# Kernel optimization log

Hardware: AMD Instinct MI355X
Metric: run time of the kernel (lower is better)

## Reference

```python
import jax, jax.numpy as jnp
import numpy as np

N = 50000      # nodes
E = 800000     # edges (before self-loops)
IN = 128       # in_channels
HID = 32       # hidden_channels per head
H = 4          # in_head
OUT = 40       # out_channels
OH = 1         # out_head
NEG = 0.2      # GATConv default negative_slope
EPS = 1e-5     # BatchNorm eps
SKIP = 0.5     # skip_coefficient


def setup_inputs() -> dict:
    key = jax.random.key(0)
    ks = jax.random.split(key, 24)
    s = 0.1
    f32 = jnp.float32
    return dict(
        x=jax.random.normal(ks[0], (N, IN), dtype=f32),
        W0=jax.random.normal(ks[1], (H * HID, IN), dtype=f32) * s,
        as0=jax.random.normal(ks[2], (H, HID), dtype=f32) * s,
        ad0=jax.random.normal(ks[3], (H, HID), dtype=f32) * s,
        b0=jnp.zeros((H * HID,), f32),
        g0=jnp.ones((H * HID,), f32),
        be0=jnp.zeros((H * HID,), f32),
        W1=jax.random.normal(ks[4], (H * HID, H * HID), dtype=f32) * s,
        as1=jax.random.normal(ks[5], (H, HID), dtype=f32) * s,
        ad1=jax.random.normal(ks[6], (H, HID), dtype=f32) * s,
        b1=jnp.zeros((H * HID,), f32),
        g1=jnp.ones((H * HID,), f32),
        be1=jnp.zeros((H * HID,), f32),
        W2=jax.random.normal(ks[7], (OH * OUT, H * HID), dtype=f32) * s,
        as2=jax.random.normal(ks[8], (OH, OUT), dtype=f32) * s,
        ad2=jax.random.normal(ks[9], (OH, OUT), dtype=f32) * s,
        b2=jnp.zeros((OH * OUT,), f32),
        edge_index=jax.random.randint(ks[10], (2, E), 0, N, dtype=jnp.int64),
    )


def gat_layer(x, src, dst, W, a_s, a_d, b, heads, ch):
    # PyG GATConv (concat=True): per-head linear, edge LeakyReLU attention,
    # softmax over incoming edges per destination node, scatter-add aggregate.
    n = x.shape[0]
    h = (x @ W.T).reshape(n, heads, ch)            # [N,H,C]
    al_s = jnp.einsum('nhc,hc->nh', h, a_s)        # [N,H]
    al_d = jnp.einsum('nhc,hc->nh', h, a_d)
    e = jax.nn.leaky_relu(al_s[src] + al_d[dst], NEG)   # [Etot,H]
    m = jax.ops.segment_max(e, dst, num_segments=n)     # per-dst max (stable softmax)
    ex = jnp.exp(e - m[dst])
    denom = jax.ops.segment_sum(ex, dst, num_segments=n)
    alpha = ex / denom[dst]                              # [Etot,H]
    out = jax.ops.segment_sum(alpha[:, :, None] * h[src], dst, num_segments=n)
    return out.reshape(n, heads * ch) + b


def batchnorm(x, g, b):
    # BatchNorm1d, batch-statistics form
    mu = x.mean(0)
    var = x.var(0)
    return (x - mu) * jax.lax.rsqrt(var + EPS) * g + b


def reference(x, W0, as0, ad0, b0, g0, be0, W1, as1, ad1, b1, g1, be1,
              W2, as2, ad2, b2, edge_index):
    loops = jnp.arange(N, dtype=edge_index.dtype)   # GATConv add_self_loops=True
    src = jnp.concatenate([edge_index[0], loops])
    dst = jnp.concatenate([edge_index[1], loops])
    h = jax.nn.relu(batchnorm(gat_layer(x, src, dst, W0, as0, ad0, b0, H, HID), g0, be0))
    skip = h
    h = gat_layer(h, src, dst, W1, as1, ad1, b1, H, HID)
    h = jax.nn.relu(batchnorm(h, g1, be1) + SKIP * skip)
    return gat_layer(h, src, dst, W2, as2, ad2, b2, OH, OUT)
```

## Files before the change

### kernel.cpp

```cpp
#include <hip/hip_runtime.h>
#include <hip/hip_bf16.h>
#include <stdint.h>

#define N_NODES 50000
#define N_EDGES 800000
#define TOT_EDGES (N_EDGES + N_NODES)
#define DIM 128
#define NEG 0.2f
#define BN_EPS 1e-5f
#define SKIPC 0.5f
#define NB 196
#define BCAP 6144

typedef __attribute__((ext_vector_type(8))) short short8;
typedef __attribute__((ext_vector_type(4))) float f32x4;

__device__ inline float bf2f(__hip_bfloat16 v) { return __bfloat162float(v); }
__device__ inline float u16f(unsigned short u) { return __uint_as_float(((unsigned int)u) << 16); }
__device__ inline unsigned short f2bu(float f) {
    __hip_bfloat16 b = __float2bfloat16(f);
    return *(unsigned short*)&b;
}
__device__ inline void fma8(float* acc, float ex, uint4 u) {
    acc[0] += ex * u16f((unsigned short)(u.x & 0xFFFFu));
    acc[1] += ex * u16f((unsigned short)(u.x >> 16));
    acc[2] += ex * u16f((unsigned short)(u.y & 0xFFFFu));
    acc[3] += ex * u16f((unsigned short)(u.y >> 16));
    acc[4] += ex * u16f((unsigned short)(u.z & 0xFFFFu));
    acc[5] += ex * u16f((unsigned short)(u.z >> 16));
    acc[6] += ex * u16f((unsigned short)(u.w & 0xFFFFu));
    acc[7] += ex * u16f((unsigned short)(u.w >> 16));
}
__device__ inline unsigned int pk2(float a, float b) {
    return (unsigned int)f2bu(a) | ((unsigned int)f2bu(b) << 16);
}

__global__ void zero_out_k(unsigned short* out, int n) {
    int g = blockIdx.x * 256 + threadIdx.x;
    if (g < n) out[g] = 0;
}

__global__ void fdetect_k(const unsigned int* __restrict__ w0, int* __restrict__ fflag) {
    __shared__ int cs;
    if (threadIdx.x == 0) cs = 0;
    __syncthreads();
    unsigned int w = w0[threadIdx.x];
    float v0 = u16f((unsigned short)(w & 0xFFFFu));
    float a = fabsf(v0);
    int sane = (a < 2.0f && (a > 1e-20f || v0 == 0.0f)) ? 1 : 0;
    atomicAdd(&cs, sane);
    __syncthreads();
    if (threadIdx.x == 0) fflag[0] = (cs >= 128) ? 1 : 0;
}

__global__ __launch_bounds__(256) void binA_k(const int* __restrict__ ei,
                                              int* __restrict__ bcnt,
                                              unsigned int* __restrict__ pairs) {
    __shared__ int cnt[NB], base[NB], cur[NB];
    __shared__ int sf;
    int t = threadIdx.x;
    if (t == 0) sf = 0;
    for (int i = t; i < NB; i += 256) cnt[i] = 0;
    __syncthreads();
    if (t < 16 && ei[2 * t + 1] != 0) atomicOr(&sf, 1);
    __syncthreads();
    int f = (sf == 0);
    int b0 = blockIdx.x * 4096;
    unsigned int pk[16];
    int bk[16];
    #pragma unroll
    for (int j = 0; j < 16; ++j) {
        int g = b0 + j * 256 + t;
        bk[j] = -1;
        if (g < N_EDGES) {
            int s, d;
            if (f) { s = ei[2 * g]; d = ei[2 * (N_EDGES + g)]; }
            else   { s = ei[g];     d = ei[N_EDGES + g]; }
            if ((unsigned)d < N_NODES && (unsigned)s < N_NODES) {
                bk[j] = d >> 8;
                pk[j] = (unsigned int)s | ((unsigned int)(d & 255) << 16);
                atomicAdd(&cnt[bk[j]], 1);
            }
        }
    }
    __syncthreads();
    if (t < NB) {
        int c = cnt[t];
        base[t] = c ? atomicAdd(&bcnt[t], c) : 0;
        cur[t] = 0;
    }
    __syncthreads();
    #pragma unroll
    for (int j = 0; j < 16; ++j) {
        if (bk[j] >= 0) {
            int off = base[bk[j]] + atomicAdd(&cur[bk[j]], 1);
            if (off < BCAP) pairs[(size_t)bk[j] * BCAP + off] = pk[j];
        }
    }
}

__global__ __launch_bounds__(256) void bucketscan_k(const int* __restrict__ bcnt,
                                                    int* __restrict__ bbase,
                                                    int* __restrict__ row_ptr) {
    __shared__ int sm[256];
    int t = threadIdx.x;
    int v = 0;
    if (t < NB) {
        int nn = min(256, N_NODES - t * 256);
        v = min(bcnt[t], BCAP) + nn;
    }
    sm[t] = v;
    __syncthreads();
    for (int off = 1; off < 256; off <<= 1) {
        int x = (t >= off) ? sm[t - off] : 0;
        __syncthreads();
        sm[t] += x;
        __syncthreads();
    }
    if (t < NB) bbase[t] = sm[t] - v;
    if (t == 255) row_ptr[N_NODES] = sm[255];
}

__global__ __launch_bounds__(256) void binB_k(const int* __restrict__ bcnt,
                                              const int* __restrict__ bbase,
                                              const unsigned int* __restrict__ pairs,
                                              int* __restrict__ row_ptr,
                                              int* __restrict__ ssrc) {
    __shared__ int cntL[256], scanL[256], curL[256];
    int b = blockIdx.x, t = threadIdx.x;
    int n0 = b * 256;
    int nn = min(256, N_NODES - n0);
    int cnt_b = min(bcnt[b], BCAP);
    const unsigned int* P = pairs + (size_t)b * BCAP;
    cntL[t] = (t < nn) ? 1 : 0;
    __syncthreads();
    for (int i = t; i < cnt_b; i += 256)
        atomicAdd(&cntL[P[i] >> 16], 1);
    __syncthreads();
    int v = cntL[t];
    scanL[t] = v;
    __syncthreads();
    for (int off = 1; off < 256; off <<= 1) {
        int x = (t >= off) ? scanL[t - off] : 0;
        __syncthreads();
        scanL[t] += x;
        __syncthreads();
    }
    int excl = scanL[t] - v;
    int gbase = bbase[b];
    if (t < nn) row_ptr[n0 + t] = gbase + excl;
    curL[t] = excl;
    __syncthreads();
    if (t < nn) {
        int pos = atomicAdd(&curL[t], 1);
        ssrc[gbase + pos] = n0 + t;
    }
    for (int i = t; i < cnt_b; i += 256) {
        unsigned int p = P[i];
        int pos = atomicAdd(&curL[p >> 16], 1);
        ssrc[gbase + pos] = (int)(p & 0xFFFFu);
    }
}

struct PrepJobs { const void* src[13]; float* dst[13]; int n[13]; };
__global__ __launch_bounds__(256) void wcvt_k(const void* __restrict__ W0,
                                              const void* __restrict__ W1,
                                              const void* __restrict__ W2,
                                              unsigned short* __restrict__ Wb0,
                                              unsigned short* __restrict__ Wb1,
                                              unsigned short* __restrict__ Wb2,
                                              PrepJobs jobs,
                                              const int* __restrict__ fflag) {
    int f = fflag[0];
    int b = blockIdx.x;
    if (b < 148) {
        int g = b * 256 + threadIdx.x;
        const void* W; unsigned short* Wb; int idx;
        if (g < 16384)        { W = W0; Wb = Wb0; idx = g; }
        else if (g < 32768)   { W = W1; Wb = Wb1; idx = g - 16384; }
        else if (g < 37888)   { W = W2; Wb = Wb2; idx = g - 32768; }
        else return;
        if (f) Wb[idx] = ((const unsigned short*)W)[idx];
        else   Wb[idx] = f2bu(((const float*)W)[idx]);
    } else {
        int j = b - 148;
        int n = jobs.n[j];
        const void* s = jobs.src[j];
        float* d = jobs.dst[j];
        for (int i = threadIdx.x; i < n; i += 256)
            d[i] = f ? bf2f(((const __hip_bfloat16*)s)[i]) : ((const float*)s)[i];
    }
}

__global__ __launch_bounds__(256) void wext_k(unsigned short* __restrict__ Wb0,
                                              unsigned short* __restrict__ Wb1,
                                              unsigned short* __restrict__ Wb2,
                                              const float* __restrict__ pAs0, const float* __restrict__ pAd0,
                                              const float* __restrict__ pAs1, const float* __restrict__ pAd1,
                                              const float* __restrict__ pAs2, const float* __restrict__ pAd2) {
    int g = blockIdx.x * 256 + threadIdx.x;
    if (g < 2048) {
        int layer = g >> 10;
        int gi = g & 1023;
        int rowq = gi >> 7;
        int k = gi & 127;
        int hh = rowq & 3, dir = rowq >> 2;
        unsigned short* Wb = layer ? Wb1 : Wb0;
        const float* p = layer ? (dir ? pAd1 : pAs1) : (dir ? pAd0 : pAs0);
        float v = 0.f;
        #pragma unroll
        for (int c = 0; c < 32; ++c)
            v += p[hh * 32 + c] * u16f(Wb[(size_t)(hh * 32 + c) * 128 + k]);
        Wb[(size_t)(128 + dir * 4 + hh) * 128 + k] = f2bu(v);
    } else if (g < 2304) {
        int gi = g - 2048;
        int dir = gi >> 7;
        int k = gi & 127;
        const float* p = dir ? pAd2 : pAs2;
        float v = 0.f;
        #pragma unroll
        for (int c = 0; c < 40; ++c)
            v += p[c] * u16f(Wb2[(size_t)c * 128 + k]);
        Wb2[(size_t)(40 + dir) * 128 + k] = f2bu(v);
    }
}

template<int MT, int MV, int ALBASE, int NH, bool BF16IN>
__device__ inline void mfma_body(const unsigned short* __restrict__ Xb,
                                 const float* __restrict__ Xf,
                                 const unsigned short* __restrict__ Wb,
                                 unsigned short* __restrict__ Y,
                                 float* __restrict__ als, float* __restrict__ ald, int n) {
    const int MROWS = ALBASE + 2 * NH;
    int wave = (blockIdx.x * blockDim.x + threadIdx.x) >> 6;
    int r0 = wave * 16;
    if (r0 >= n) return;
    int lane = threadIdx.x & 63;
    int m = lane & 15, quad = lane >> 4;
    f32x4 acc[MT];
    #pragma unroll
    for (int t = 0; t < MT; ++t) acc[t] = (f32x4){0.f, 0.f, 0.f, 0.f};
    int arow = min(r0 + m, n - 1);

    #pragma unroll
    for (int kc = 0; kc < 4; ++kc) {
        int k0 = kc * 32 + quad * 8;
        short8 a;
        if (BF16IN) {
            a = *(const short8*)(Xb + (size_t)arow * 128 + k0);
        } else {
            const float* xp = Xf + (size_t)arow * 128 + k0;
            float4 x0 = *(const float4*)xp;
            float4 x1 = *(const float4*)(xp + 4);
            a[0] = (short)f2bu(x0.x); a[1] = (short)f2bu(x0.y);
            a[2] = (short)f2bu(x0.z); a[3] = (short)f2bu(x0.w);
            a[4] = (short)f2bu(x1.x); a[5] = (short)f2bu(x1.y);
            a[6] = (short)f2bu(x1.z); a[7] = (short)f2bu(x1.w);
        }
        #pragma unroll
        for (int t = 0; t < MT; ++t) {
            int col = t * 16 + m;
            short8 b;
            if (col < MROWS) b = *(const short8*)(Wb + (size_t)col * 128 + k0);
            else             b = (short8){0,0,0,0,0,0,0,0};
            acc[t] = __builtin_amdgcn_mfma_f32_16x16x32_bf16(a, b, acc[t], 0, 0, 0);
        }
    }

    #pragma unroll
    for (int t = 0; t < MT; ++t) {
        int col = t * 16 + m;
        #pragma unroll
        for (int r = 0; r < 4; ++r) {
            int row = r0 + quad * 4 + r;
            if (row >= n) continue;
            if (col < MV) {
                Y[(size_t)row * MV + col] = f2bu(acc[t][r]);
            } else if (col < ALBASE + NH) {
                als[row * NH + (col - ALBASE)] = acc[t][r];
            } else if (col < ALBASE + 2 * NH) {
                ald[row * NH + (col - ALBASE - NH)] = acc[t][r];
            }
        }
    }
}

__global__ __launch_bounds__(256) void mfma_x_k(const void* __restrict__ X,
                                                const unsigned short* __restrict__ Wb,
                                                unsigned short* __restrict__ Y,
                                                float* __restrict__ als, float* __restrict__ ald,
                                                int n, const int* __restrict__ fflag) {
    if (fflag[0]) mfma_body<9, 128, 128, 4, true>((const unsigned short*)X, nullptr, Wb, Y, als, ald, n);
    else          mfma_body<9, 128, 128, 4, false>(nullptr, (const float*)X, Wb, Y, als, ald, n);
}

__global__ __launch_bounds__(256) void mfma_b_k(const unsigned short* __restrict__ X,
                                                const unsigned short* __restrict__ Wb,
                                                unsigned short* __restrict__ Y,
                                                float* __restrict__ als, float* __restrict__ ald, int n) {
    mfma_body<9, 128, 128, 4, true>(X, nullptr, Wb, Y, als, ald, n);
}

__global__ __launch_bounds__(256) void mfma_b40_k(const unsigned short* __restrict__ X,
                                                  const unsigned short* __restrict__ Wb,
                                                  unsigned short* __restrict__ Y,
                                                  float* __restrict__ als, float* __restrict__ ald, int n) {
    mfma_body<3, 40, 40, 1, true>(X, nullptr, Wb, Y, als, ald, n);
}

template<int H, int C, int LPG, int CPL, bool FINAL>
__global__ __launch_bounds__(256) void agg4_k(const unsigned short* __restrict__ hbuf,
                                              const float* __restrict__ als,
                                              const float* __restrict__ ald,
                                              const float* __restrict__ bias,
                                              const int* __restrict__ row_ptr,
                                              const int* __restrict__ ssrc,
                                              void* __restrict__ out,
                                              const int* __restrict__ fflag, int n) {
    const int HC = H * C;
    const int G = 64 / LPG;
    const int NV = CPL / 8;
    int gw = (blockIdx.x * blockDim.x + threadIdx.x) >> 6;
    if (gw >= n) return;
    int lane = threadIdx.x & 63;
    int grp = lane / LPG;
    int sl  = lane % LPG;
    int c0 = sl * CPL;
    bool act = c0 < HC;
    int hl = act ? (c0 / C) : 0;
    int d = gw;
    int beg = row_ptr[d], end = row_ptr[d + 1];
    float adh = ald[d * H + hl];

    float denom = 0.f;
    float acc[CPL];
    #pragma unroll
    for (int j = 0; j < CPL; ++j) acc[j] = 0.f;

    int i0 = beg + grp;
    bool h0 = i0 < end;
    bool h1 = (i0 + G) < end;
    float al0 = 0.f, al1 = 0.f;
    uint4 u0[NV], u1[NV];
    if (h0) {
        int s = ssrc[i0];
        al0 = als[s * H + hl];
        if (act) {
            const uint4* hp = (const uint4*)(hbuf + (size_t)s * HC + c0);
            #pragma unroll
            for (int v = 0; v < NV; ++v) u0[v] = hp[v];
        }
    }
    if (h1) {
        int s = ssrc[i0 + G];
        al1 = als[s * H + hl];
        if (act) {
            const uint4* hp = (const uint4*)(hbuf + (size_t)s * HC + c0);
            #pragma unroll
            for (int v = 0; v < NV; ++v) u1[v] = hp[v];
        }
    }
    int inext = i0 + 2 * G;

    while (h0) {
        bool h2 = inext < end;
        float al2 = 0.f;
        uint4 u2[NV];
        if (h2) {
            int s = ssrc[inext];
            al2 = als[s * H + hl];
            if (act) {
                const uint4* hp = (const uint4*)(hbuf + (size_t)s * HC + c0);
                #pragma unroll
                for (int v = 0; v < NV; ++v) u2[v] = hp[v];
            }
        }
        float t = al0 + adh;
        t = t > 0.f ? t : NEG * t;
        float ex = __expf(t);
        denom += ex;
        if (act) {
            #pragma unroll
            for (int v = 0; v < NV; ++v) fma8(acc + v * 8, ex, u0[v]);
        }
        h0 = h1; al0 = al1;
        #pragma unroll
        for (int v = 0; v < NV; ++v) u0[v] = u1[v];
        h1 = h2; al1 = al2;
        #pragma unroll
        for (int v = 0; v < NV; ++v) u1[v] = u2[v];
        inext += G;
    }

    #pragma unroll
    for (int off = LPG; off < 64; off <<= 1) {
        denom += __shfl_xor(denom, off, 64);
        #pragma unroll
        for (int j = 0; j < CPL; ++j) acc[j] += __shfl_xor(acc[j], off, 64);
    }

    if (grp == 0 && act) {
        float inv = 1.f / denom;
        float vals[CPL];
        #pragma unroll
        for (int j = 0; j < CPL; ++j) vals[j] = acc[j] * inv + bias[c0 + j];
        if (FINAL && !fflag[0]) {
            float* of = (float*)out + (size_t)d * HC + c0;
            #pragma unroll
            for (int j = 0; j < CPL; ++j) of[j] = vals[j];
        } else {
            unsigned short* ob = (unsigned short*)out + (size_t)d * HC + c0;
            #pragma unroll
            for (int v = 0; v < NV; ++v) {
                uint4 pk;
                pk.x = pk2(vals[v * 8 + 0], vals[v * 8 + 1]);
                pk.y = pk2(vals[v * 8 + 2], vals[v * 8 + 3]);
                pk.z = pk2(vals[v * 8 + 4], vals[v * 8 + 5]);
                pk.w = pk2(vals[v * 8 + 6], vals[v * 8 + 7]);
                *(uint4*)(ob + v * 8) = pk;
            }
        }
    }
}

__global__ __launch_bounds__(256) void bn_stats_k(const unsigned short* __restrict__ x,
                                                  float* __restrict__ sum,
                                                  float* __restrict__ sumsq, int n) {
    __shared__ float ss[256], sq[256];
    int t = threadIdx.x;
    int c = t & 127, half = t >> 7;
    float s = 0.f, s2 = 0.f;
    for (int r = blockIdx.x * 2 + half; r < n; r += gridDim.x * 2) {
        float v = u16f(x[(size_t)r * 128 + c]);
        s += v; s2 += v * v;
    }
    ss[t] = s; sq[t] = s2;
    __syncthreads();
    if (t < 128) {
        s = ss[t] + ss[t + 128];
        s2 = sq[t] + sq[t + 128];
        atomicAdd(&sum[c], s);
        atomicAdd(&sumsq[c], s2);
    }
}

__global__ void bn_apply_k(const unsigned short* __restrict__ x,
                           const unsigned short* __restrict__ skip,
                           unsigned short* __restrict__ y,
                           const float* __restrict__ sum, const float* __restrict__ sumsq,
                           const float* __restrict__ g, const float* __restrict__ be, int n) {
    int gid = blockIdx.x * 256 + threadIdx.x;
    if (gid >= n * 32) return;
    int e0 = gid * 4;
    int c0 = e0 & 127;
    const float invN = 1.f / (float)N_NODES;
    float4 gg = *(const float4*)(g + c0);
    float4 bb = *(const float4*)(be + c0);
    float4 sm = *(const float4*)(sum + c0);
    float4 sq = *(const float4*)(sumsq + c0);
    ushort4 xv = *(const ushort4*)(x + e0);
    float vx[4] = { u16f(xv.x), u16f(xv.y), u16f(xv.z), u16f(xv.w) };
    float mg[4] = { gg.x, gg.y, gg.z, gg.w };
    float mb[4] = { bb.x, bb.y, bb.z, bb.w };
    float ms[4] = { sm.x, sm.y, sm.z, sm.w };
    float mq[4] = { sq.x, sq.y, sq.z, sq.w };
    float sk[4] = { 0.f, 0.f, 0.f, 0.f };
    if (skip) {
        ushort4 sv = *(const ushort4*)(skip + e0);
        sk[0] = u16f(sv.x); sk[1] = u16f(sv.y); sk[2] = u16f(sv.z); sk[3] = u16f(sv.w);
    }
    unsigned short o[4];
    #pragma unroll
    for (int j = 0; j < 4; ++j) {
        float mean = ms[j] * invN;
        float var = fmaxf(mq[j] * invN - mean * mean, 0.f);
        float inv = rsqrtf(var + BN_EPS);
        float v = (vx[j] - mean) * inv * mg[j] + mb[j];
        if (skip) v += SKIPC * sk[j];
        o[j] = f2bu(fmaxf(v, 0.f));
    }
    *(ushort4*)(y + e0) = make_ushort4(o[0], o[1], o[2], o[3]);
}

extern "C" void kernel_launch(void* const* d_in, const int* in_sizes, int n_in,
                              void* d_out, int out_size, void* d_ws, size_t ws_size,
                              hipStream_t stream) {
    const void* x   = d_in[0];
    const void* W0  = d_in[1];
    const void* as0 = d_in[2];
    const void* ad0 = d_in[3];
    const void* b0  = d_in[4];
    const void* g0  = d_in[5];
    const void* be0 = d_in[6];
    const void* W1  = d_in[7];
    const void* as1 = d_in[8];
    const void* ad1 = d_in[9];
    const void* b1  = d_in[10];
    const void* g1  = d_in[11];
    const void* be1 = d_in[12];
    const void* W2  = d_in[13];
    const void* as2 = d_in[14];
    const void* ad2 = d_in[15];
    const void* b2  = d_in[16];
    const int* ei = (const int*)d_in[17];

    char* w = (char*)d_ws;
    size_t off = 0;
    auto alloc = [&](size_t bytes) -> void* {
        void* p = w + off;
        off = (off + bytes + 255) & ~(size_t)255;
        return p;
    };
    unsigned short* hAgg = (unsigned short*)alloc((size_t)N_NODES * 128 * 2);
    unsigned short* hbf  = (unsigned short*)alloc((size_t)N_NODES * 128 * 2);
    unsigned short* hS   = (unsigned short*)alloc((size_t)N_NODES * 128 * 2);
    unsigned short* hI   = (unsigned short*)alloc((size_t)N_NODES * 128 * 2);
    float* als = (float*)alloc((size_t)N_NODES * 4 * 4);
    float* ald = (float*)alloc((size_t)N_NODES * 4 * 4);
    unsigned short* Wb0 = (unsigned short*)alloc((size_t)136 * 128 * 2);
    unsigned short* Wb1 = (unsigned short*)alloc((size_t)136 * 128 * 2);
    unsigned short* Wb2 = (unsigned short*)alloc((size_t)42 * 128 * 2);
    float* prm = (float*)alloc(2048 * 4);
    int* zreg = (int*)alloc((size_t)(NB + 512) * 4);
    int* bcnt = zreg;
    float* bn0 = (float*)(zreg + NB);
    float* bn1 = bn0 + 256;
    int* row_ptr = (int*)alloc((size_t)(N_NODES + 1) * 4);
    int* ssrc    = (int*)alloc((size_t)TOT_EDGES * 4);
    unsigned int* pairs = (unsigned int*)alloc((size_t)NB * BCAP * 4);
    int* bbase   = (int*)alloc((size_t)NB * 4);
    int* fflag   = (int*)alloc(256);

    float* pAs0 = prm + 0,   * pAd0 = prm + 128,  * pB0 = prm + 256;
    float* pG0  = prm + 384, * pBe0 = prm + 512;
    float* pAs1 = prm + 640, * pAd1 = prm + 768,  * pB1 = prm + 896;
    float* pG1  = prm + 1024,* pBe1 = prm + 1152;
    float* pAs2 = prm + 1280,* pAd2 = prm + 1320, * pB2 = prm + 1360;

    if (off > ws_size) {
        zero_out_k<<<(out_size + 255) / 256, 256, 0, stream>>>((unsigned short*)d_out, out_size);
        return;
    }

    const int MB = (((N_NODES + 15) / 16) + 3) / 4;
    const int AB = (N_NODES * 64 + 255) / 256;
    const int XB4 = (N_NODES * 32 + 255) / 256;

    fdetect_k<<<1, 256, 0, stream>>>((const unsigned int*)W0, fflag);
    hipMemsetAsync(zreg, 0, (size_t)(NB + 512) * 4, stream);
    binA_k<<<(N_EDGES + 4095) / 4096, 256, 0, stream>>>(ei, bcnt, pairs);
    bucketscan_k<<<1, 256, 0, stream>>>(bcnt, bbase, row_ptr);
    binB_k<<<NB, 256, 0, stream>>>(bcnt, bbase, pairs, row_ptr, ssrc);

    PrepJobs jobs;
    const void* srcs[13] = { as0, ad0, b0, g0, be0, as1, ad1, b1, g1, be1, as2, ad2, b2 };
    float* dsts[13] = { pAs0, pAd0, pB0, pG0, pBe0, pAs1, pAd1, pB1, pG1, pBe1, pAs2, pAd2, pB2 };
    int ns[13] = { 128,128,128,128,128, 128,128,128,128,128, 40,40,40 };
    for (int i = 0; i < 13; ++i) { jobs.src[i] = srcs[i]; jobs.dst[i] = dsts[i]; jobs.n[i] = ns[i]; }
    wcvt_k<<<161, 256, 0, stream>>>(W0, W1, W2, Wb0, Wb1, Wb2, jobs, fflag);
    wext_k<<<9, 256, 0, stream>>>(Wb0, Wb1, Wb2, pAs0, pAd0, pAs1, pAd1, pAs2, pAd2);

    mfma_x_k<<<MB, 256, 0, stream>>>(x, Wb0, hbf, als, ald, N_NODES, fflag);
    agg4_k<4, 32, 8, 16, false><<<AB, 256, 0, stream>>>(hbf, als, ald, pB0, row_ptr, ssrc, hAgg, fflag, N_NODES);
    bn_stats_k<<<256, 256, 0, stream>>>(hAgg, bn0, bn0 + 128, N_NODES);
    bn_apply_k<<<XB4, 256, 0, stream>>>(hAgg, nullptr, hS, bn0, bn0 + 128, pG0, pBe0, N_NODES);

    mfma_b_k<<<MB, 256, 0, stream>>>(hS, Wb1, hbf, als, ald, N_NODES);
    agg4_k<4, 32, 8, 16, false><<<AB, 256, 0, stream>>>(hbf, als, ald, pB1, row_ptr, ssrc, hAgg, fflag, N_NODES);
    bn_stats_k<<<256, 256, 0, stream>>>(hAgg, bn1, bn1 + 128, N_NODES);
    bn_apply_k<<<XB4, 256, 0, stream>>>(hAgg, hS, hI, bn1, bn1 + 128, pG1, pBe1, N_NODES);

    mfma_b40_k<<<MB, 256, 0, stream>>>(hI, Wb2, hbf, als, ald, N_NODES);
    agg4_k<1, 40, 8, 8, true><<<AB, 256, 0, stream>>>(hbf, als, ald, pB2, row_ptr, ssrc, d_out, fflag, N_NODES);
}
```

Before: 365.6 us.

## Fuse BatchNorm apply and skip into following MFMA matmul prologues

Removes the standalone bn_apply kernels. A tiny kernel precomputes per-channel scale/shift, and the next layer's MFMA kernel applies BN, ReLU and the skip connection while loading its A operand. Layer-0 activations are recomputed from the aggregated buffer in the layer-2 prologue instead of being stored. The fdetect kernel is also folded into wcvt_k, with each block recomputing the flag. This saves two full-size activation write/read round trips and one launch, at the cost of extra ALU work in the matmul prologues.

After: 366.7 us. No clear change (+0.3%).

```diff
diff --git a/kernel.cpp b/kernel.cpp
--- a/kernel.cpp
+++ b/kernel.cpp
@@ -38,19 +38,6 @@
 __global__ void zero_out_k(unsigned short* out, int n) {
     int g = blockIdx.x * 256 + threadIdx.x;
     if (g < n) out[g] = 0;
-}
-
-__global__ void fdetect_k(const unsigned int* __restrict__ w0, int* __restrict__ fflag) {
-    __shared__ int cs;
-    if (threadIdx.x == 0) cs = 0;
-    __syncthreads();
-    unsigned int w = w0[threadIdx.x];
-    float v0 = u16f((unsigned short)(w & 0xFFFFu));
-    float a = fabsf(v0);
-    int sane = (a < 2.0f && (a > 1e-20f || v0 == 0.0f)) ? 1 : 0;
-    atomicAdd(&cs, sane);
-    __syncthreads();
-    if (threadIdx.x == 0) fflag[0] = (cs >= 128) ? 1 : 0;
 }
 
 __global__ __launch_bounds__(256) void binA_k(const int* __restrict__ ei,
@@ -170,11 +157,22 @@
                                               unsigned short* __restrict__ Wb1,
                                               unsigned short* __restrict__ Wb2,
                                               PrepJobs jobs,
-                                              const int* __restrict__ fflag) {
-    int f = fflag[0];
+                                              int* __restrict__ fflag) {
+    __shared__ int cs;
+    int t = threadIdx.x;
+    if (t == 0) cs = 0;
+    __syncthreads();
+    unsigned int wv = ((const unsigned int*)W0)[t];
+    float v0 = u16f((unsigned short)(wv & 0xFFFFu));
+    float av = fabsf(v0);
+    if (av < 2.0f && (av > 1e-20f || v0 == 0.0f)) atomicAdd(&cs, 1);
+    __syncthreads();
+    int f = (cs >= 128);
+    if (blockIdx.x == 0 && t == 0) fflag[0] = f;
+
     int b = blockIdx.x;
     if (b < 148) {
-        int g = b * 256 + threadIdx.x;
+        int g = b * 256 + t;
         const void* W; unsigned short* Wb; int idx;
         if (g < 16384)        { W = W0; Wb = Wb0; idx = g; }
         else if (g < 32768)   { W = W1; Wb = Wb1; idx = g - 16384; }
@@ -187,7 +185,7 @@
         int n = jobs.n[j];
         const void* s = jobs.src[j];
         float* d = jobs.dst[j];
-        for (int i = threadIdx.x; i < n; i += 256)
+        for (int i = t; i < n; i += 256)
             d[i] = f ? bf2f(((const __hip_bfloat16*)s)[i]) : ((const float*)s)[i];
     }
 }
@@ -225,48 +223,42 @@
     }
 }
 
-template<int MT, int MV, int ALBASE, int NH, bool BF16IN>
-__device__ inline void mfma_body(const unsigned short* __restrict__ Xb,
-                                 const float* __restrict__ Xf,
+__global__ void bn_coef_k(const float* __restrict__ sums,
+                          const float* __restrict__ g, const float* __restrict__ be,
+                          float* __restrict__ coef) {
+    int t = threadIdx.x;
+    if (t >= 128) return;
+    const float invN = 1.f / (float)N_NODES;
+    float mean = sums[t] * invN;
+    float var = fmaxf(sums[128 + t] * invN - mean * mean, 0.f);
+    float sc = g[t] * rsqrtf(var + BN_EPS);
+    coef[t] = sc;
+    coef[128 + t] = be[t] - mean * sc;
+}
+
+template<int MT, int MV, int ALBASE, int NH>
+__device__ inline void mfma_core(short8 (&aF)[4],
                                  const unsigned short* __restrict__ Wb,
                                  unsigned short* __restrict__ Y,
-                                 float* __restrict__ als, float* __restrict__ ald, int n) {
+                                 float* __restrict__ als, float* __restrict__ ald,
+                                 int r0, int lane, int n) {
     const int MROWS = ALBASE + 2 * NH;
-    int wave = (blockIdx.x * blockDim.x + threadIdx.x) >> 6;
-    int r0 = wave * 16;
-    if (r0 >= n) return;
-    int lane = threadIdx.x & 63;
     int m = lane & 15, quad = lane >> 4;
     f32x4 acc[MT];
     #pragma unroll
     for (int t = 0; t < MT; ++t) acc[t] = (f32x4){0.f, 0.f, 0.f, 0.f};
-    int arow = min(r0 + m, n - 1);
-
     #pragma unroll
     for (int kc = 0; kc < 4; ++kc) {
         int k0 = kc * 32 + quad * 8;
-        short8 a;
-        if (BF16IN) {
-            a = *(const short8*)(Xb + (size_t)arow * 128 + k0);
-        } else {
-            const float* xp = Xf + (size_t)arow * 128 + k0;
-            float4 x0 = *(const float4*)xp;
-            float4 x1 = *(const float4*)(xp + 4);
-            a[0] = (short)f2bu(x0.x); a[1] = (short)f2bu(x0.y);
-            a[2] = (short)f2bu(x0.z); a[3] = (short)f2bu(x0.w);
-            a[4] = (short)f2bu(x1.x); a[5] = (short)f2bu(x1.y);
-            a[6] = (short)f2bu(x1.z); a[7] = (short)f2bu(x1.w);
-        }
         #pragma unroll
         for (int t = 0; t < MT; ++t) {
             int col = t * 16 + m;
             short8 b;
             if (col < MROWS) b = *(const short8*)(Wb + (size_t)col * 128 + k0);
             else             b = (short8){0,0,0,0,0,0,0,0};
-            acc[t] = __builtin_amdgcn_mfma_f32_16x16x32_bf16(a, b, acc[t], 0, 0, 0);
-        }
-    }
-
+            acc[t] = __builtin_amdgcn_mfma_f32_16x16x32_bf16(aF[kc], b, acc[t], 0, 0, 0);
+        }
+    }
     #pragma unroll
     for (int t = 0; t < MT; ++t) {
         int col = t * 16 + m;
@@ -290,22 +282,108 @@
                                                 unsigned short* __restrict__ Y,
                                                 float* __restrict__ als, float* __restrict__ ald,
                                                 int n, const int* __restrict__ fflag) {
-    if (fflag[0]) mfma_body<9, 128, 128, 4, true>((const unsigned short*)X, nullptr, Wb, Y, als, ald, n);
-    else          mfma_body<9, 128, 128, 4, false>(nullptr, (const float*)X, Wb, Y, als, ald, n);
-}
-
-__global__ __launch_bounds__(256) void mfma_b_k(const unsigned short* __restrict__ X,
-                                                const unsigned short* __restrict__ Wb,
-                                                unsigned short* __restrict__ Y,
-                                                float* __restrict__ als, float* __restrict__ ald, int n) {
-    mfma_body<9, 128, 128, 4, true>(X, nullptr, Wb, Y, als, ald, n);
-}
-
-__global__ __launch_bounds__(256) void mfma_b40_k(const unsigned short* __restrict__ X,
+    int wave = (blockIdx.x * blockDim.x + threadIdx.x) >> 6;
+    int r0 = wave * 16;
+    if (r0 >= n) return;
+    int lane = threadIdx.x & 63;
+    int arow = min(r0 + (lane & 15), n - 1);
+    int quad = lane >> 4;
+    short8 aF[4];
+    if (fflag[0]) {
+        #pragma unroll
+        for (int kc = 0; kc < 4; ++kc)
+            aF[kc] = *(const short8*)((const unsigned short*)X + (size_t)arow * 128 + kc * 32 + quad * 8);
+    } else {
+        #pragma unroll
+        for (int kc = 0; kc < 4; ++kc) {
+            const float* xp = (const float*)X + (size_t)arow * 128 + kc * 32 + quad * 8;
+            float4 x0 = *(const float4*)xp;
+            float4 x1 = *(const float4*)(xp + 4);
+            aF[kc][0] = (short)f2bu(x0.x); aF[kc][1] = (short)f2bu(x0.y);
+            aF[kc][2] = (short)f2bu(x0.z); aF[kc][3] = (short)f2bu(x0.w);
+            aF[kc][4] = (short)f2bu(x1.x); aF[kc][5] = (short)f2bu(x1.y);
+            aF[kc][6] = (short)f2bu(x1.z); aF[kc][7] = (short)f2bu(x1.w);
+        }
+    }
+    mfma_core<9, 128, 128, 4>(aF, Wb, Y, als, ald, r0, lane, n);
+}
+
+__global__ __launch_bounds__(256) void mfma_bn1_k(const unsigned short* __restrict__ hA0,
+                                                  const float* __restrict__ coef0,
                                                   const unsigned short* __restrict__ Wb,
                                                   unsigned short* __restrict__ Y,
-                                                  float* __restrict__ als, float* __restrict__ ald, int n) {
-    mfma_body<3, 40, 40, 1, true>(X, nullptr, Wb, Y, als, ald, n);
+                                                  float* __restrict__ als, float* __restrict__ ald,
+                                                  int n) {
+    int wave = (blockIdx.x * blockDim.x + threadIdx.x) >> 6;
+    int r0 = wave * 16;
+    if (r0 >= n) return;
+    int lane = threadIdx.x & 63;
+    int arow = min(r0 + (lane & 15), n - 1);
+    int quad = lane >> 4;
+    short8 aF[4];
+    #pragma unroll
+    for (int kc = 0; kc < 4; ++kc) {
+        int k0 = kc * 32 + quad * 8;
+        uint4 ux = *(const uint4*)(hA0 + (size_t)arow * 128 + k0);
+        float4 scA = *(const float4*)(coef0 + k0);
+        float4 scB = *(const float4*)(coef0 + k0 + 4);
+        float4 shA = *(const float4*)(coef0 + 128 + k0);
+        float4 shB = *(const float4*)(coef0 + 128 + k0 + 4);
+        float v[8];
+        v[0] = u16f((unsigned short)(ux.x & 0xFFFFu)); v[1] = u16f((unsigned short)(ux.x >> 16));
+        v[2] = u16f((unsigned short)(ux.y & 0xFFFFu)); v[3] = u16f((unsigned short)(ux.y >> 16));
+        v[4] = u16f((unsigned short)(ux.z & 0xFFFFu)); v[5] = u16f((unsigned short)(ux.z >> 16));
+        v[6] = u16f((unsigned short)(ux.w & 0xFFFFu)); v[7] = u16f((unsigned short)(ux.w >> 16));
+        aF[kc][0] = (short)f2bu(fmaxf(scA.x * v[0] + shA.x, 0.f));
+        aF[kc][1] = (short)f2bu(fmaxf(scA.y * v[1] + shA.y, 0.f));
+        aF[kc][2] = (short)f2bu(fmaxf(scA.z * v[2] + shA.z, 0.f));
+        aF[kc][3] = (short)f2bu(fmaxf(scA.w * v[3] + shA.w, 0.f));
+        aF[kc][4] = (short)f2bu(fmaxf(scB.x * v[4] + shB.x, 0.f));
+        aF[kc][5] = (short)f2bu(fmaxf(scB.y * v[5] + shB.y, 0.f));
+        aF[kc][6] = (short)f2bu(fmaxf(scB.z * v[6] + shB.z, 0.f));
+        aF[kc][7] = (short)f2bu(fmaxf(scB.w * v[7] + shB.w, 0.f));
+    }
+    mfma_core<9, 128, 128, 4>(aF, Wb, Y, als, ald, r0, lane, n);
+}
+
+__global__ __launch_bounds__(256) void mfma_bn2_k(const unsigned short* __restrict__ hA1,
+                                                  const unsigned short* __restrict__ hA0,
+                                                  const float* __restrict__ coef1,
+                                                  const float* __restrict__ coef0,
+                                                  const unsigned short* __restrict__ Wb,
+                                                  unsigned short* __restrict__ Y,
+                                                  float* __restrict__ als, float* __restrict__ ald,
+                                                  int n) {
+    int wave = (blockIdx.x * blockDim.x + threadIdx.x) >> 6;
+    int r0 = wave * 16;
+    if (r0 >= n) return;
+    int lane = threadIdx.x & 63;
+    int arow = min(r0 + (lane & 15), n - 1);
+    int quad = lane >> 4;
+    short8 aF[4];
+    #pragma unroll
+    for (int kc = 0; kc < 4; ++kc) {
+        int k0 = kc * 32 + quad * 8;
+        uint4 u1 = *(const uint4*)(hA1 + (size_t)arow * 128 + k0);
+        uint4 u0 = *(const uint4*)(hA0 + (size_t)arow * 128 + k0);
+        float v1[8], v0[8];
+        v1[0] = u16f((unsigned short)(u1.x & 0xFFFFu)); v1[1] = u16f((unsigned short)(u1.x >> 16));
+        v1[2] = u16f((unsigned short)(u1.y & 0xFFFFu)); v1[3] = u16f((unsigned short)(u1.y >> 16));
+        v1[4] = u16f((unsigned short)(u1.z & 0xFFFFu)); v1[5] = u16f((unsigned short)(u1.z >> 16));
+        v1[6] = u16f((unsigned short)(u1.w & 0xFFFFu)); v1[7] = u16f((unsigned short)(u1.w >> 16));
+        v0[0] = u16f((unsigned short)(u0.x & 0xFFFFu)); v0[1] = u16f((unsigned short)(u0.x >> 16));
+        v0[2] = u16f((unsigned short)(u0.y & 0xFFFFu)); v0[3] = u16f((unsigned short)(u0.y >> 16));
+        v0[4] = u16f((unsigned short)(u0.z & 0xFFFFu)); v0[5] = u16f((unsigned short)(u0.z >> 16));
+        v0[6] = u16f((unsigned short)(u0.w & 0xFFFFu)); v0[7] = u16f((unsigned short)(u0.w >> 16));
+        #pragma unroll
+        for (int j = 0; j < 8; ++j) {
+            int c = k0 + j;
+            float s0 = fmaxf(coef0[c] * v0[j] + coef0[128 + c], 0.f);
+            float v = coef1[c] * v1[j] + coef1[128 + c] + SKIPC * s0;
+            aF[kc][j] = (short)f2bu(fmaxf(v, 0.f));
+        }
+    }
+    mfma_core<3, 40, 40, 1>(aF, Wb, Y, als, ald, r0, lane, n);
 }
 
 template<int H, int C, int LPG, int CPL, bool FINAL>
@@ -444,44 +522,6 @@
     }
 }
 
-__global__ void bn_apply_k(const unsigned short* __restrict__ x,
-                           const unsigned short* __restrict__ skip,
-                           unsigned short* __restrict__ y,
-                           const float* __restrict__ sum, const float* __restrict__ sumsq,
-                           const float* __restrict__ g, const float* __restrict__ be, int n) {
-    int gid = blockIdx.x * 256 + threadIdx.x;
-    if (gid >= n * 32) return;
-    int e0 = gid * 4;
-    int c0 = e0 & 127;
-    const float invN = 1.f / (float)N_NODES;
-    float4 gg = *(const float4*)(g + c0);
-    float4 bb = *(const float4*)(be + c0);
-    float4 sm = *(const float4*)(sum + c0);
-    float4 sq = *(const float4*)(sumsq + c0);
-    ushort4 xv = *(const ushort4*)(x + e0);
-    float vx[4] = { u16f(xv.x), u16f(xv.y), u16f(xv.z), u16f(xv.w) };
-    float mg[4] = { gg.x, gg.y, gg.z, gg.w };
-    float mb[4] = { bb.x, bb.y, bb.z, bb.w };
-    float ms[4] = { sm.x, sm.y, sm.z, sm.w };
-    float mq[4] = { sq.x, sq.y, sq.z, sq.w };
-    float sk[4] = { 0.f, 0.f, 0.f, 0.f };
-    if (skip) {
-        ushort4 sv = *(const ushort4*)(skip + e0);
-        sk[0] = u16f(sv.x); sk[1] = u16f(sv.y); sk[2] = u16f(sv.z); sk[3] = u16f(sv.w);
-    }
-    unsigned short o[4];
-    #pragma unroll
-    for (int j = 0; j < 4; ++j) {
-        float mean = ms[j] * invN;
-        float var = fmaxf(mq[j] * invN - mean * mean, 0.f);
-        float inv = rsqrtf(var + BN_EPS);
-        float v = (vx[j] - mean) * inv * mg[j] + mb[j];
-        if (skip) v += SKIPC * sk[j];
-        o[j] = f2bu(fmaxf(v, 0.f));
-    }
-    *(ushort4*)(y + e0) = make_ushort4(o[0], o[1], o[2], o[3]);
-}
-
 extern "C" void kernel_launch(void* const* d_in, const int* in_sizes, int n_in,
                               void* d_out, int out_size, void* d_ws, size_t ws_size,
                               hipStream_t stream) {
@@ -511,16 +551,17 @@
         off = (off + bytes + 255) & ~(size_t)255;
         return p;
     };
-    unsigned short* hAgg = (unsigned short*)alloc((size_t)N_NODES * 128 * 2);
-    unsigned short* hbf  = (unsigned short*)alloc((size_t)N_NODES * 128 * 2);
-    unsigned short* hS   = (unsigned short*)alloc((size_t)N_NODES * 128 * 2);
-    unsigned short* hI   = (unsigned short*)alloc((size_t)N_NODES * 128 * 2);
+    unsigned short* hAgg0 = (unsigned short*)alloc((size_t)N_NODES * 128 * 2);
+    unsigned short* hAgg1 = (unsigned short*)alloc((size_t)N_NODES * 128 * 2);
+    unsigned short* hbf   = (unsigned short*)alloc((size_t)N_NODES * 128 * 2);
     float* als = (float*)alloc((size_t)N_NODES * 4 * 4);
     float* ald = (float*)alloc((size_t)N_NODES * 4 * 4);
     unsigned short* Wb0 = (unsigned short*)alloc((size_t)136 * 128 * 2);
     unsigned short* Wb1 = (unsigned short*)alloc((size_t)136 * 128 * 2);
     unsigned short* Wb2 = (unsigned short*)alloc((size_t)42 * 128 * 2);
     float* prm = (float*)alloc(2048 * 4);
+    float* coef0 = (float*)alloc(256 * 4);
+    float* coef1 = (float*)alloc(256 * 4);
     int* zreg = (int*)alloc((size_t)(NB + 512) * 4);
     int* bcnt = zreg;
     float* bn0 = (float*)(zreg + NB);
@@ -544,9 +585,7 @@
 
     const int MB = (((N_NODES + 15) / 16) + 3) / 4;
     const int AB = (N_NODES * 64 + 255) / 256;
-    const int XB4 = (N_NODES * 32 + 255) / 256;
-
-    fdetect_k<<<1, 256, 0, stream>>>((const unsigned int*)W0, fflag);
+
     hipMemsetAsync(zreg, 0, (size_t)(NB + 512) * 4, stream);
     binA_k<<<(N_EDGES + 4095) / 4096, 256, 0, stream>>>(ei, bcnt, pairs);
     bucketscan_k<<<1, 256, 0, stream>>>(bcnt, bbase, row_ptr);
@@ -561,15 +600,15 @@
     wext_k<<<9, 256, 0, stream>>>(Wb0, Wb1, Wb2, pAs0, pAd0, pAs1, pAd1, pAs2, pAd2);
 
     mfma_x_k<<<MB, 256, 0, stream>>>(x, Wb0, hbf, als, ald, N_NODES, fflag);
-    agg4_k<4, 32, 8, 16, false><<<AB, 256, 0, stream>>>(hbf, als, ald, pB0, row_ptr, ssrc, hAgg, fflag, N_NODES);
-    bn_stats_k<<<256, 256, 0, stream>>>(hAgg, bn0, bn0 + 128, N_NODES);
-    bn_apply_k<<<XB4, 256, 0, stream>>>(hAgg, nullptr, hS, bn0, bn0 + 128, pG0, pBe0, N_NODES);
-
-    mfma_b_k<<<MB, 256, 0, stream>>>(hS, Wb1, hbf, als, ald, N_NODES);
-    agg4_k<4, 32, 8, 16, false><<<AB, 256, 0, stream>>>(hbf, als, ald, pB1, row_ptr, ssrc, hAgg, fflag, N_NODES);
-    bn_stats_k<<<256, 256, 0, stream>>>(hAgg, bn1, bn1 + 128, N_NODES);
-    bn_apply_k<<<XB4, 256, 0, stream>>>(hAgg, hS, hI, bn1, bn1 + 128, pG1, pBe1, N_NODES);
-
-    mfma_b40_k<<<MB, 256, 0, stream>>>(hI, Wb2, hbf, als, ald, N_NODES);
+    agg4_k<4, 32, 8, 16, false><<<AB, 256, 0, stream>>>(hbf, als, ald, pB0, row_ptr, ssrc, hAgg0, fflag, N_NODES);
+    bn_stats_k<<<256, 256, 0, stream>>>(hAgg0, bn0, bn0 + 128, N_NODES);
+    bn_coef_k<<<1, 128, 0, stream>>>(bn0, pG0, pBe0, coef0);
+
+    mfma_bn1_k<<<MB, 256, 0, stream>>>(hAgg0, coef0, Wb1, hbf, als, ald, N_NODES);
+    agg4_k<4, 32, 8, 16, false><<<AB, 256, 0, stream>>>(hbf, als, ald, pB1, row_ptr, ssrc, hAgg1, fflag, N_NODES);
+    bn_stats_k<<<256, 256, 0, stream>>>(hAgg1, bn1, bn1 + 128, N_NODES);
+    bn_coef_k<<<1, 128, 0, stream>>>(bn1, pG1, pBe1, coef1);
+
+    mfma_bn2_k<<<MB, 256, 0, stream>>>(hAgg1, hAgg0, coef1, coef0, Wb2, hbf, als, ald, N_NODES);
     agg4_k<1, 40, 8, 8, true><<<AB, 256, 0, stream>>>(hbf, als, ald, pB2, row_ptr, ssrc, d_out, fflag, N_NODES);
 }
```
